# Kernel optimization log

Measured on AMD Instinct MI355X. Metric: run time of the kernel, lower is better.

## Reference

```python
import jax, jax.numpy as jnp
import numpy as np

TAU = 0.5
EPS = 1e-12  # F.normalize eps


def _l2_normalize(z):
    n = jnp.linalg.norm(z, axis=1, keepdims=True)
    return z / jnp.maximum(n, EPS)


def _semi_loss(a, b):
    # a, b: [N, d], already raw embeddings; normalize then exp(sim/tau)
    an = _l2_normalize(a)
    bn = _l2_normalize(b)
    refl = jnp.exp(jnp.matmul(an, an.T) / TAU)      # [N, N]
    between = jnp.exp(jnp.matmul(an, bn.T) / TAU)   # [N, N]
    pos = jnp.diagonal(between)
    denom = refl.sum(axis=1) + between.sum(axis=1) - jnp.diagonal(refl)
    return -jnp.log(pos / denom)


def setup_inputs() -> dict:
    key = jax.random.key(0)
    k1, k2 = jax.random.split(key)
    z1 = jax.random.normal(k1, (8192, 256), dtype=jnp.float32)
    z2 = jax.random.normal(k2, (8192, 256), dtype=jnp.float32)
    return {"z1": z1, "z2": z2, "mean": 1}


def reference(z1, z2, mean):
    l1 = _semi_loss(z1, z2)
    l2 = _semi_loss(z2, z1)
    ret = (l1 + l2) * 0.5
    return ret.mean() if mean else ret.sum()
```

## Files before the change

### kernel.cpp

```cpp
#include <hip/hip_runtime.h>
#include <hip/hip_bf16.h>
#include <hip/hip_fp8.h>

#define N_ROWS 8192
#define NZ 16384
#define DIM 256
#define TAU_INV 2.0f
#define BT 128
#define NTILE 128
#define NTRI (NTILE * (NTILE + 1) / 2)
#define NCHUNK 16

typedef float f32x4 __attribute__((ext_vector_type(4)));
typedef long lx2 __attribute__((ext_vector_type(2)));

__global__ __launch_bounds__(256) void normalize_kernel(
    const float* __restrict__ z1, const float* __restrict__ z2,
    unsigned char* __restrict__ Z8, float* __restrict__ pos)
{
    const int tid = threadIdx.x;
    const int wave = tid >> 6;
    const int lane = tid & 63;
    const int row = blockIdx.x * 4 + wave;

    const float4 a = ((const float4*)(z1 + (size_t)row * DIM))[lane];
    const float4 b = ((const float4*)(z2 + (size_t)row * DIM))[lane];

    auto wsum = [&](float v) -> float {
        #pragma unroll
        for (int m = 1; m < 64; m <<= 1) v += __shfl_xor(v, m, 64);
        return v;
    };

    const float na2 = wsum(a.x*a.x + a.y*a.y + a.z*a.z + a.w*a.w);
    const float nb2 = wsum(b.x*b.x + b.y*b.y + b.z*b.z + b.w*b.w);
    const float sa = 16.0f / sqrtf(na2);
    const float sb = 16.0f / sqrtf(nb2);

    const float av[4] = {a.x*sa, a.y*sa, a.z*sa, a.w*sa};
    const float bv[4] = {b.x*sb, b.y*sb, b.z*sb, b.w*sb};
    unsigned char pa[4], pb[4];
    float qd = 0.0f;
    #pragma unroll
    for (int k = 0; k < 4; ++k) {
        __hip_fp8_e4m3 qa(av[k]);
        __hip_fp8_e4m3 qb(bv[k]);
        pa[k] = qa.__x; pb[k] = qb.__x;
        qd += float(qa) * float(qb);
    }
    const int g  = (lane >> 1) & 7;
    const int pp = ((g & 3) << 1) | (g >> 2);
    const int off = (lane >> 4) * 64 + pp * 8 + (lane & 1) * 4;
    *(uchar4*)(Z8 + (size_t)row * DIM + off) = *(uchar4*)pa;
    *(uchar4*)(Z8 + (size_t)(N_ROWS + row) * DIM + off) = *(uchar4*)pb;

    qd = wsum(qd);
    if (lane == 0) pos[row] = qd * 0.00390625f;
}

template <bool TWO_STAGE>
__global__ __launch_bounds__(256, 4) void gram_kernel(
    const unsigned char* __restrict__ Z,
    float* __restrict__ part, float* __restrict__ S)
{
    const int bid = (blockIdx.x & 7) * (NTRI / 8) + (blockIdx.x >> 3);
    int ti = (int)((257.0f - sqrtf(66049.0f - 8.0f * (float)bid)) * 0.5f);
    ti = ti < 0 ? 0 : (ti > 127 ? 127 : ti);
    while (ti * (257 - ti) / 2 > bid) --ti;
    while ((ti + 1) * (256 - ti) / 2 <= bid) ++ti;
    const int tj = ti + (bid - ti * (257 - ti) / 2);
    const bool diag = (ti == tj);

    __shared__ unsigned char Ls[32768];

    const int tid  = threadIdx.x;
    const int wave = tid >> 6;
    const int lane = tid & 63;
    const int wr = wave >> 1, wc = wave & 1;
    const int lm = lane & 15, lq = lane >> 4;

    const int r8 = lane >> 3;
    const int pg = lane & 7;
    const int G0 = pg ^ (r8 >> 1);
    const int dlt = 64 - ((G0 & 4) << 5);
    const unsigned char* pAE =
        Z + (size_t)(ti * BT + wave * 32 + r8) * DIM + (G0 << 4);
    const unsigned char* pBE =
        Z + (size_t)(tj * BT + wave * 32 + r8) * DIM + (G0 << 4);
    const unsigned char* pAO = pAE + dlt;
    const unsigned char* pBO = pBE + dlt;

    const int s0 = (lq ^ (lm >> 1)) << 4;
    const int s1 = s0 ^ 64;
    const unsigned char* LA0 = Ls + wr * 8192 + lm * 128 + s0;
    const unsigned char* LA1 = Ls + wr * 8192 + lm * 128 + s1;
    const unsigned char* LB0 = Ls + 16384 + wc * 8192 + lm * 128 + s0;
    const unsigned char* LB1 = Ls + 16384 + wc * 8192 + lm * 128 + s1;

    f32x4 acc[4][4] = {};

    #pragma unroll
    for (int kh = 0; kh < 2; ++kh) {
        if (kh) __syncthreads();
        #pragma unroll
        for (int c = 0; c < 4; ++c) {
            const int ld = (wave * 4 + c) * 1024;
            const unsigned char* ga = ((c & 1) ? pAO : pAE) + c * 2048 + kh * 128;
            const unsigned char* gb = ((c & 1) ? pBO : pBE) + c * 2048 + kh * 128;
            __builtin_amdgcn_global_load_lds(
                (const __attribute__((address_space(1))) void*)ga,
                (__attribute__((address_space(3))) void*)(Ls + ld), 16, 0, 0);
            __builtin_amdgcn_global_load_lds(
                (const __attribute__((address_space(1))) void*)gb,
                (__attribute__((address_space(3))) void*)(Ls + 16384 + ld), 16, 0, 0);
        }
        __syncthreads();

        lx2 aP[4], bP[4];
        #pragma unroll
        for (int f = 0; f < 4; ++f) {
            aP[f] = *(const lx2*)(LA0 + f * 2048);
            bP[f] = *(const lx2*)(LB0 + f * 2048);
        }
        #pragma unroll
        for (int fr = 0; fr < 4; ++fr)
            #pragma unroll
            for (int fc = 0; fc < 4; ++fc) {
                acc[fr][fc] = __builtin_amdgcn_mfma_f32_16x16x32_fp8_fp8(
                    aP[fr].x, bP[fc].x, acc[fr][fc], 0, 0, 0);
                acc[fr][fc] = __builtin_amdgcn_mfma_f32_16x16x32_fp8_fp8(
                    aP[fr].y, bP[fc].y, acc[fr][fc], 0, 0, 0);
            }
        #pragma unroll
        for (int f = 0; f < 4; ++f) {
            aP[f] = *(const lx2*)(LA1 + f * 2048);
            bP[f] = *(const lx2*)(LB1 + f * 2048);
        }
        #pragma unroll
        for (int fr = 0; fr < 4; ++fr)
            #pragma unroll
            for (int fc = 0; fc < 4; ++fc) {
                acc[fr][fc] = __builtin_amdgcn_mfma_f32_16x16x32_fp8_fp8(
                    aP[fr].x, bP[fc].x, acc[fr][fc], 0, 0, 0);
                acc[fr][fc] = __builtin_amdgcn_mfma_f32_16x16x32_fp8_fp8(
                    aP[fr].y, bP[fc].y, acc[fr][fc], 0, 0, 0);
            }
    }

    const float SC = 2.8853900817779268f / 256.0f;
    #pragma unroll
    for (int fr = 0; fr < 4; ++fr)
        #pragma unroll
        for (int fc = 0; fc < 4; ++fc)
            #pragma unroll
            for (int r = 0; r < 4; ++r)
                acc[fr][fc][r] = exp2f(acc[fr][fc][r] * SC);

    if (diag) {
        #pragma unroll
        for (int fr = 0; fr < 4; ++fr) {
            const int gi = wr * 64 + fr * 16 + lq * 4;
            #pragma unroll
            for (int fc = 0; fc < 4; ++fc) {
                const int gj = wc * 64 + fc * 16 + lm;
                #pragma unroll
                for (int r = 0; r < 4; ++r)
                    if (gj <= gi + r) acc[fr][fc][r] = 0.0f;
            }
        }
    }

    float* dst = TWO_STAGE ? (part + (size_t)bid * 512) : nullptr;

    #pragma unroll
    for (int fr = 0; fr < 4; ++fr)
        #pragma unroll
        for (int r = 0; r < 4; ++r) {
            float s = acc[fr][0][r] + acc[fr][1][r] + acc[fr][2][r] + acc[fr][3][r];
            s += __shfl_xor(s, 1, 64);
            s += __shfl_xor(s, 2, 64);
            s += __shfl_xor(s, 4, 64);
            s += __shfl_xor(s, 8, 64);
            if (lm == 0) {
                const int rr = wr * 64 + fr * 16 + lq * 4 + r;
                if (TWO_STAGE) dst[wc * 128 + rr] = s;
                else atomicAdd(&S[ti * BT + rr], s);
            }
        }
    #pragma unroll
    for (int fc = 0; fc < 4; ++fc) {
        float s = 0.0f;
        #pragma unroll
        for (int fr = 0; fr < 4; ++fr)
            #pragma unroll
            for (int r = 0; r < 4; ++r) s += acc[fr][fc][r];
        s += __shfl_xor(s, 16, 64);
        s += __shfl_xor(s, 32, 64);
        if (lq == 0) {
            const int cc = wc * 64 + fc * 16 + lm;
            if (TWO_STAGE) dst[256 + wr * 128 + cc] = s;
            else atomicAdd(&S[tj * BT + cc], s);
        }
    }
}

__global__ __launch_bounds__(256) void reduce_kernel(
    const float* __restrict__ part, float* __restrict__ S2,
    float* __restrict__ out)
{
    const int chunk = blockIdx.y;
    const int tid = threadIdx.x;
    const int r = blockIdx.x * 256 + tid;
    const int tr = r >> 7, rr = r & 127;
    const int baseRow = tr * (257 - tr) / 2;
    const int cntRow = 2 * (128 - tr);

    if (chunk == 0 && r == 0) out[0] = 0.0f;

    float s = 0.0f;
    for (int m = chunk; m < 258; m += NCHUNK) {
        size_t addr;
        if (m < cntRow) {
            const int bb = baseRow + (m >> 1);
            addr = (size_t)bb * 512 + (m & 1) * 128 + rr;
        } else {
            const int m2 = m - cntRow;
            const int tiq = m2 >> 1;
            const int bb = tiq * (257 - tiq) / 2 + (tr - tiq);
            addr = (size_t)bb * 512 + 256 + (m2 & 1) * 128 + rr;
        }
        s += part[addr];
    }
    S2[(size_t)chunk * NZ + r] = s;
}

__global__ __launch_bounds__(256) void loss2_kernel(
    const float* __restrict__ S2, const float* __restrict__ pos,
    float* __restrict__ out)
{
    const int i = blockIdx.x * 256 + threadIdx.x;
    float den1 = 0.0f, den2 = 0.0f;
    #pragma unroll
    for (int c = 0; c < NCHUNK; ++c) {
        den1 += S2[(size_t)c * NZ + i];
        den2 += S2[(size_t)c * NZ + N_ROWS + i];
    }
    float v = 0.5f * (logf(den1) + logf(den2)) - TAU_INV * pos[i];

    __shared__ float red[4];
    #pragma unroll
    for (int m = 1; m < 64; m <<= 1) v += __shfl_xor(v, m, 64);
    if ((threadIdx.x & 63) == 0) red[threadIdx.x >> 6] = v;
    __syncthreads();
    if (threadIdx.x == 0)
        atomicAdd(out, (red[0] + red[1] + red[2] + red[3]) * (1.0f / N_ROWS));
}

__global__ __launch_bounds__(256) void loss_kernel(
    const float* __restrict__ S, const float* __restrict__ pos,
    float* __restrict__ out)
{
    const int i = blockIdx.x * 256 + threadIdx.x;
    float v = 0.5f * (logf(S[i]) + logf(S[N_ROWS + i])) - TAU_INV * pos[i];

    __shared__ float red[4];
    #pragma unroll
    for (int m = 1; m < 64; m <<= 1) v += __shfl_xor(v, m, 64);
    if ((threadIdx.x & 63) == 0) red[threadIdx.x >> 6] = v;
    __syncthreads();
    if (threadIdx.x == 0)
        atomicAdd(out, (red[0] + red[1] + red[2] + red[3]) * (1.0f / N_ROWS));
}

extern "C" void kernel_launch(void* const* d_in, const int* in_sizes, int n_in,
                              void* d_out, int out_size, void* d_ws, size_t ws_size,
                              hipStream_t stream)
{
    const float* z1 = (const float*)d_in[0];
    const float* z2 = (const float*)d_in[1];
    float* out = (float*)d_out;

    char* ws = (char*)d_ws;
    unsigned char* Z8 = (unsigned char*)ws;
    float* pos  = (float*)(ws + 4194304);
    float* S2   = (float*)(ws + 4227072);
    float* part = (float*)(ws + 5275648);
    const size_t need = 5275648 + (size_t)NTRI * 512 * 4;

    normalize_kernel<<<N_ROWS / 4, 256, 0, stream>>>(z1, z2, Z8, pos);

    if (ws_size >= need) {
        gram_kernel<true><<<NTRI, 256, 0, stream>>>(Z8, part, nullptr);
        dim3 rg(NZ / 256, NCHUNK);
        reduce_kernel<<<rg, 256, 0, stream>>>(part, S2, out);
        loss2_kernel<<<N_ROWS / 256, 256, 0, stream>>>(S2, pos, out);
    } else {
        hipMemsetAsync(S2, 0, NZ * sizeof(float), stream);
        hipMemsetAsync(out, 0, sizeof(float), stream);
        gram_kernel<false><<<NTRI, 256, 0, stream>>>(Z8, nullptr, S2);
        loss_kernel<<<N_ROWS / 256, 256, 0, stream>>>(S2, pos, out);
    }
}
```

Measured before the change: 159.6 us.

## Fuse partial reduction with loss, fold exp scale into normalization

```diff
diff --git a/kernel.cpp b/kernel.cpp
--- a/kernel.cpp
+++ b/kernel.cpp
@@ -5,20 +5,22 @@
 #define N_ROWS 8192
 #define NZ 16384
 #define DIM 256
-#define TAU_INV 2.0f
 #define BT 128
 #define NTILE 128
 #define NTRI (NTILE * (NTILE + 1) / 2)
-#define NCHUNK 16
 
 typedef float f32x4 __attribute__((ext_vector_type(4)));
 typedef long lx2 __attribute__((ext_vector_type(2)));
 
 __global__ __launch_bounds__(256) void normalize_kernel(
     const float* __restrict__ z1, const float* __restrict__ z2,
-    unsigned char* __restrict__ Z8, float* __restrict__ pos)
+    unsigned char* __restrict__ Z8, float* __restrict__ pos,
+    float* __restrict__ S, float* __restrict__ out)
 {
     const int tid = threadIdx.x;
+    if (blockIdx.x < 64) S[blockIdx.x * 256 + tid] = 0.0f;
+    if (blockIdx.x == 0 && tid == 0) out[0] = 0.0f;
+
     const int wave = tid >> 6;
     const int lane = tid & 63;
     const int row = blockIdx.x * 4 + wave;
@@ -34,8 +36,9 @@
 
     const float na2 = wsum(a.x*a.x + a.y*a.y + a.z*a.z + a.w*a.w);
     const float nb2 = wsum(b.x*b.x + b.y*b.y + b.z*b.z + b.w*b.w);
-    const float sa = 16.0f / sqrtf(na2);
-    const float sb = 16.0f / sqrtf(nb2);
+    const float ALPHA = 1.6986436f;
+    const float sa = ALPHA / sqrtf(na2);
+    const float sb = ALPHA / sqrtf(nb2);
 
     const float av[4] = {a.x*sa, a.y*sa, a.z*sa, a.w*sa};
     const float bv[4] = {b.x*sb, b.y*sb, b.z*sb, b.w*sb};
@@ -55,7 +58,7 @@
     *(uchar4*)(Z8 + (size_t)(N_ROWS + row) * DIM + off) = *(uchar4*)pb;
 
     qd = wsum(qd);
-    if (lane == 0) pos[row] = qd * 0.00390625f;
+    if (lane == 0) pos[row] = qd;
 }
 
 template <bool TWO_STAGE>
@@ -147,14 +150,13 @@
             }
     }
 
-    const float SC = 2.8853900817779268f / 256.0f;
     #pragma unroll
     for (int fr = 0; fr < 4; ++fr)
         #pragma unroll
         for (int fc = 0; fc < 4; ++fc)
             #pragma unroll
             for (int r = 0; r < 4; ++r)
-                acc[fr][fc][r] = exp2f(acc[fr][fc][r] * SC);
+                acc[fr][fc][r] = exp2f(acc[fr][fc][r]);
 
     if (diag) {
         #pragma unroll
@@ -204,21 +206,20 @@
     }
 }
 
-__global__ __launch_bounds__(256) void reduce_kernel(
-    const float* __restrict__ part, float* __restrict__ S2,
+__global__ __launch_bounds__(1024) void reduce_loss_kernel(
+    const float* __restrict__ part, const float* __restrict__ pos,
     float* __restrict__ out)
 {
-    const int chunk = blockIdx.y;
     const int tid = threadIdx.x;
-    const int r = blockIdx.x * 256 + tid;
-    const int tr = r >> 7, rr = r & 127;
-    const int baseRow = tr * (257 - tr) / 2;
-    const int cntRow = 2 * (128 - tr);
-
-    if (chunk == 0 && r == 0) out[0] = 0.0f;
+    const int rr = tid & 127;
+    const int sl = (tid >> 7) & 3;
+    const int p  = tid >> 9;
+    const int t  = blockIdx.x + p * 64;
+    const int baseRow = t * (257 - t) / 2;
+    const int cntRow = 2 * (128 - t);
 
     float s = 0.0f;
-    for (int m = chunk; m < 258; m += NCHUNK) {
+    for (int m = sl; m < 258; m += 4) {
         size_t addr;
         if (m < cntRow) {
             const int bb = baseRow + (m >> 1);
@@ -226,26 +227,38 @@
         } else {
             const int m2 = m - cntRow;
             const int tiq = m2 >> 1;
-            const int bb = tiq * (257 - tiq) / 2 + (tr - tiq);
+            const int bb = tiq * (257 - tiq) / 2 + (t - tiq);
             addr = (size_t)bb * 512 + 256 + (m2 & 1) * 128 + rr;
         }
         s += part[addr];
     }
-    S2[(size_t)chunk * NZ + r] = s;
-}
-
-__global__ __launch_bounds__(256) void loss2_kernel(
-    const float* __restrict__ S2, const float* __restrict__ pos,
+
+    __shared__ float L[2][4][128];
+    __shared__ float red[2];
+    L[p][sl][rr] = s;
+    __syncthreads();
+
+    if (tid < 128) {
+        const float den1 = L[0][0][rr] + L[0][1][rr] + L[0][2][rr] + L[0][3][rr];
+        const float den2 = L[1][0][rr] + L[1][1][rr] + L[1][2][rr] + L[1][3][rr];
+        const int i = blockIdx.x * 128 + rr;
+        float v = 0.5f * (logf(den1) + logf(den2)) - 0.69314718056f * pos[i];
+        #pragma unroll
+        for (int mm = 1; mm < 64; mm <<= 1) v += __shfl_xor(v, mm, 64);
+        if ((tid & 63) == 0) red[tid >> 6] = v;
+    }
+    __syncthreads();
+    if (tid == 0)
+        atomicAdd(out, (red[0] + red[1]) * (1.0f / N_ROWS));
+}
+
+__global__ __launch_bounds__(256) void loss_kernel(
+    const float* __restrict__ S, const float* __restrict__ pos,
     float* __restrict__ out)
 {
     const int i = blockIdx.x * 256 + threadIdx.x;
-    float den1 = 0.0f, den2 = 0.0f;
-    #pragma unroll
-    for (int c = 0; c < NCHUNK; ++c) {
-        den1 += S2[(size_t)c * NZ + i];
-        den2 += S2[(size_t)c * NZ + N_ROWS + i];
-    }
-    float v = 0.5f * (logf(den1) + logf(den2)) - TAU_INV * pos[i];
+    float v = 0.5f * (logf(S[i]) + logf(S[N_ROWS + i]))
+              - 0.69314718056f * pos[i];
 
     __shared__ float red[4];
     #pragma unroll
@@ -256,22 +269,6 @@
         atomicAdd(out, (red[0] + red[1] + red[2] + red[3]) * (1.0f / N_ROWS));
 }
 
-__global__ __launch_bounds__(256) void loss_kernel(
-    const float* __restrict__ S, const float* __restrict__ pos,
-    float* __restrict__ out)
-{
-    const int i = blockIdx.x * 256 + threadIdx.x;
-    float v = 0.5f * (logf(S[i]) + logf(S[N_ROWS + i])) - TAU_INV * pos[i];
-
-    __shared__ float red[4];
-    #pragma unroll
-    for (int m = 1; m < 64; m <<= 1) v += __shfl_xor(v, m, 64);
-    if ((threadIdx.x & 63) == 0) red[threadIdx.x >> 6] = v;
-    __syncthreads();
-    if (threadIdx.x == 0)
-        atomicAdd(out, (red[0] + red[1] + red[2] + red[3]) * (1.0f / N_ROWS));
-}
-
 extern "C" void kernel_launch(void* const* d_in, const int* in_sizes, int n_in,
                               void* d_out, int out_size, void* d_ws, size_t ws_size,
                               hipStream_t stream)
@@ -283,21 +280,17 @@
     char* ws = (char*)d_ws;
     unsigned char* Z8 = (unsigned char*)ws;
     float* pos  = (float*)(ws + 4194304);
-    float* S2   = (float*)(ws + 4227072);
-    float* part = (float*)(ws + 5275648);
-    const size_t need = 5275648 + (size_t)NTRI * 512 * 4;
-
-    normalize_kernel<<<N_ROWS / 4, 256, 0, stream>>>(z1, z2, Z8, pos);
+    float* S    = (float*)(ws + 4227072);
+    float* part = (float*)(ws + 4292608);
+    const size_t need = 4292608 + (size_t)NTRI * 512 * 4;
+
+    normalize_kernel<<<N_ROWS / 4, 256, 0, stream>>>(z1, z2, Z8, pos, S, out);
 
     if (ws_size >= need) {
         gram_kernel<true><<<NTRI, 256, 0, stream>>>(Z8, part, nullptr);
-        dim3 rg(NZ / 256, NCHUNK);
-        reduce_kernel<<<rg, 256, 0, stream>>>(part, S2, out);
-        loss2_kernel<<<N_ROWS / 256, 256, 0, stream>>>(S2, pos, out);
+        reduce_loss_kernel<<<64, 1024, 0, stream>>>(part, pos, out);
     } else {
-        hipMemsetAsync(S2, 0, NZ * sizeof(float), stream);
-        hipMemsetAsync(out, 0, sizeof(float), stream);
-        gram_kernel<false><<<NTRI, 256, 0, stream>>>(Z8, nullptr, S2);
-        loss_kernel<<<N_ROWS / 256, 256, 0, stream>>>(S2, pos, out);
-    }
-}
+        gram_kernel<false><<<NTRI, 256, 0, stream>>>(Z8, nullptr, S);
+        loss_kernel<<<N_ROWS / 256, 256, 0, stream>>>(S, pos, out);
+    }
+}
```

Result: slower. 172.5 us (+8.1%).
